# Optimization experiments

Measured on AMD Instinct MI355X. Metric: run time of the kernel, lower is better.

## Reference

```python
import jax, jax.numpy as jnp
import numpy as np

DIM = 1024
NQ = 16
NKV = 4
HD = DIM // NQ  # 64
HID = 2048
E = 8
B, S = 1, 1024
EPS = 1e-6


def rmsnorm(x, w):
    ms = jnp.mean(x * x, axis=-1, keepdims=True)
    return w * (x * jax.lax.rsqrt(ms + EPS))


def rope_tables(seq_len, head_dim):
    inv_freq = 1.0 / (10000.0 ** (jnp.arange(0, head_dim, 2, dtype=jnp.float32) / head_dim))
    t = jnp.arange(seq_len, dtype=jnp.float32)
    freqs = jnp.einsum('i,j->ij', t, inv_freq)  # [S, HD/2]
    return jnp.cos(freqs), jnp.sin(freqs)


def apply_rope(x, cos, sin):
    # x: [B, S, H, HD]; cos/sin: [S, HD/2]
    c = cos[None, :, None, :]
    s = sin[None, :, None, :]
    half = x.shape[-1] // 2
    x1, x2 = x[..., :half], x[..., half:]
    return jnp.concatenate([x1 * c - x2 * s, x1 * s + x2 * c], axis=-1)


def setup_inputs() -> dict:
    key = jax.random.key(0)
    ks = jax.random.split(key, 20)
    sc = lambda fan_in: 1.0 / np.sqrt(fan_in)
    d = {}
    d['x'] = jax.random.normal(ks[0], (B, S, DIM), dtype=jnp.float32)
    d['ln1_w'] = jnp.ones((DIM,), jnp.float32)
    d['ln2_w'] = jnp.ones((DIM,), jnp.float32)
    d['Wq'] = jax.random.normal(ks[1], (DIM, DIM), jnp.float32) * sc(DIM)
    d['bq'] = jnp.zeros((DIM,), jnp.float32)
    d['Wk'] = jax.random.normal(ks[2], (DIM, HD * NKV), jnp.float32) * sc(DIM)
    d['bk'] = jnp.zeros((HD * NKV,), jnp.float32)
    d['Wv'] = jax.random.normal(ks[3], (DIM, HD * NKV), jnp.float32) * sc(DIM)
    d['bv'] = jnp.zeros((HD * NKV,), jnp.float32)
    d['qn_w'] = jnp.ones((HD,), jnp.float32)
    d['kn_w'] = jnp.ones((HD,), jnp.float32)
    d['Wg'] = jax.random.normal(ks[4], (HD, HD), jnp.float32) * sc(HD)
    d['bg'] = jnp.zeros((HD,), jnp.float32)
    d['Wo'] = jax.random.normal(ks[5], (DIM, DIM), jnp.float32) * sc(DIM)
    d['bo'] = jnp.zeros((DIM,), jnp.float32)
    d['Wr'] = jax.random.normal(ks[6], (DIM, E), jnp.float32) * sc(DIM)
    d['br'] = jnp.zeros((E,), jnp.float32)
    d['W1'] = jax.random.normal(ks[7], (E, DIM, 2 * HID), jnp.float32) * sc(DIM)
    d['b1'] = jnp.zeros((E, 2 * HID), jnp.float32)
    d['W2'] = jax.random.normal(ks[8], (E, HID, DIM), jnp.float32) * sc(HID)
    d['b2'] = jnp.zeros((E, DIM), jnp.float32)
    return d


def _forward(x, ln1_w, ln2_w, Wq, bq, Wk, bk, Wv, bv, qn_w, kn_w, Wg, bg, Wo, bo,
             Wr, br, W1, b1, W2, b2):
    batch, seq, _ = x.shape
    cos, sin = rope_tables(seq, HD)

    # --- attention ---
    h = rmsnorm(x, ln1_w)
    q = (h @ Wq + bq).reshape(batch, seq, NQ, HD)
    k = (h @ Wk + bk).reshape(batch, seq, NKV, HD)
    v = (h @ Wv + bv).reshape(batch, seq, NKV, HD)
    q = rmsnorm(apply_rope(q, cos, sin), qn_w)
    k = rmsnorm(apply_rope(k, cos, sin), kn_w)
    rep = NQ // NKV
    k = jnp.repeat(k, rep, axis=2)  # [B,S,NQ,HD]
    v = jnp.repeat(v, rep, axis=2)
    scores = jnp.einsum('bthd,bshd->bhts', q, k) / np.sqrt(HD)
    causal = jnp.tril(jnp.ones((seq, seq), dtype=bool))
    scores = jnp.where(causal[None, None], scores, -jnp.inf)
    attn = jax.nn.softmax(scores, axis=-1)
    out = jnp.einsum('bhts,bshd->bthd', attn, v)
    gate = jax.nn.sigmoid(out @ Wg + bg)
    out = (out * gate).reshape(batch, seq, DIM)
    x = x + out @ Wo + bo

    # --- top-1 MoE (note: output is NOT scaled by router probs) ---
    h2 = rmsnorm(x, ln2_w)
    logits = h2 @ Wr + br  # [B,S,E]
    top1 = jnp.argmax(logits, axis=-1).reshape(-1)  # [T]
    xt = h2.reshape(-1, DIM)  # [T,DIM]
    # dense dispatch: run all experts, gather the chosen one
    u = jnp.einsum('td,edf->tef', xt, W1) + b1  # [T,E,2H]
    u1, u2 = u[..., :HID], u[..., HID:]
    act = u1 * jax.nn.sigmoid(u2)  # SwiGLU
    y_all = jnp.einsum('teh,ehd->ted', act, W2) + b2  # [T,E,DIM]
    y = jnp.take_along_axis(y_all, top1[:, None, None], axis=1)[:, 0, :]
    return x + y.reshape(batch, seq, DIM)


def reference(x, ln1_w, ln2_w, Wq, bq, Wk, bk, Wv, bv, qn_w, kn_w, Wg, bg, Wo, bo,
              Wr, br, W1, b1, W2, b2):
    return _forward(x, ln1_w, ln2_w, Wq, bq, Wk, bk, Wv, bv, qn_w, kn_w,
                    Wg, bg, Wo, bo, Wr, br, W1, b1, W2, b2)
```

## Files before the change

kernel.cpp:

```cpp
#include <hip/hip_runtime.h>
#include <hip/hip_bf16.h>
#include <cstddef>

#define DIM 1024
#define NQ 16
#define NKV 4
#define HD 64
#define HID 2048
#define NE 8
#define SEQ 1024
#define EPSF 1e-6f
#define MAX_TILES 24
#define GST 72

typedef __hip_bfloat16 bf16;
typedef __attribute__((ext_vector_type(8))) short short8;
typedef __attribute__((ext_vector_type(4))) float floatx4;

typedef union { short8 s; unsigned int u[4]; } s8u;

__device__ __forceinline__ unsigned int f2b(float f) {
    union { bf16 b; unsigned short s; } u;
    u.b = __float2bfloat16(f);
    return (unsigned int)u.s;
}
__device__ __forceinline__ unsigned int pk2(float a, float b) {
    return f2b(a) | (f2b(b) << 16);
}

__global__ __launch_bounds__(256) void rmsnorm_kernel(const float* __restrict__ src,
                                                      const float* __restrict__ w,
                                                      float* __restrict__ dst)
{
    int row = blockIdx.x, tid = threadIdx.x;
    __shared__ float red[256];
    float vals[4];
    float sq = 0.f;
    size_t base = (size_t)row * DIM;
    #pragma unroll
    for (int i = 0; i < 4; i++) {
        int idx = tid + i * 256;
        float v = src[base + idx];
        vals[i] = v; sq += v * v;
    }
    red[tid] = sq; __syncthreads();
    for (int s = 128; s > 0; s >>= 1) {
        if (tid < s) red[tid] += red[tid + s];
        __syncthreads();
    }
    float rs = 1.0f / sqrtf(red[0] * (1.0f / DIM) + EPSF);
    #pragma unroll
    for (int i = 0; i < 4; i++) {
        int idx = tid + i * 256;
        dst[base + idx] = w[idx] * vals[i] * rs;
    }
}

__global__ __launch_bounds__(256) void gemm_kernel(
    const float* __restrict__ A, const float* __restrict__ B, const float* __restrict__ bias,
    float* __restrict__ C, const float* __restrict__ resf,
    const int* __restrict__ perm, const int* __restrict__ tile_expert,
    int N, int K, int mode)
{
    __shared__ short As[64 * GST];
    __shared__ short Bs[64 * GST];
    int tid = threadIdx.x;
    int mbase = blockIdx.y * 64, nbase = blockIdx.x * 64;

    size_t Beoff = 0, biasoff = 0;
    if (tile_expert) {
        int e = tile_expert[blockIdx.y];
        if (e < 0) return;
        Beoff = (size_t)e * K * N;
        biasoff = (size_t)e * N;
    }

    int ar = tid >> 4, ak = (tid & 15) << 2;
    int bn = tid & 63, bkk = (tid >> 6) << 4;
    const float* BpBase = B + Beoff + (size_t)bkk * N + nbase + bn;

    int wv = tid >> 6, ln = tid & 63;
    int fm = (wv << 4) + (ln & 15);
    int fn = ln & 15;
    int fk = (ln >> 4) << 3;

    floatx4 acc[4];
    #pragma unroll
    for (int nt = 0; nt < 4; nt++)
        #pragma unroll
        for (int r = 0; r < 4; r++) acc[nt][r] = 0.f;

    float4 apre[4];
    float bpre[16];
    #pragma unroll
    for (int p = 0; p < 4; p++)
        apre[p] = *(const float4*)(A + (size_t)(mbase + (p << 4) + ar) * K + ak);
    #pragma unroll
    for (int i = 0; i < 16; i++)
        bpre[i] = BpBase[(size_t)i * N];

    for (int kt = 0; kt < K; kt += 64) {
        #pragma unroll
        for (int p = 0; p < 4; p++) {
            int m = (p << 4) + ar;
            uint2 wpk; wpk.x = pk2(apre[p].x, apre[p].y); wpk.y = pk2(apre[p].z, apre[p].w);
            *(uint2*)&As[m * GST + ak] = wpk;
        }
        {
            unsigned int u[8];
            #pragma unroll
            for (int i = 0; i < 8; i++) u[i] = pk2(bpre[2 * i], bpre[2 * i + 1]);
            *(uint4*)&Bs[bn * GST + bkk]     = make_uint4(u[0], u[1], u[2], u[3]);
            *(uint4*)&Bs[bn * GST + bkk + 8] = make_uint4(u[4], u[5], u[6], u[7]);
        }
        __syncthreads();

        int kn = kt + 64;
        if (kn < K) {
            #pragma unroll
            for (int p = 0; p < 4; p++)
                apre[p] = *(const float4*)(A + (size_t)(mbase + (p << 4) + ar) * K + kn + ak);
            const float* bp = BpBase + (size_t)kn * N;
            #pragma unroll
            for (int i = 0; i < 16; i++) bpre[i] = bp[(size_t)i * N];
        }

        #pragma unroll
        for (int ks = 0; ks < 2; ks++) {
            short8 af = *(const short8*)&As[fm * GST + (ks << 5) + fk];
            #pragma unroll
            for (int nt = 0; nt < 4; nt++) {
                short8 bf = *(const short8*)&Bs[((nt << 4) + fn) * GST + (ks << 5) + fk];
                acc[nt] = __builtin_amdgcn_mfma_f32_16x16x32_bf16(af, bf, acc[nt], 0, 0, 0);
            }
        }
        __syncthreads();
    }

    int rowb = mbase + (wv << 4) + ((ln >> 4) << 2);
    if (mode == 2) {
        int tk[4];
        #pragma unroll
        for (int r = 0; r < 4; r++) tk[r] = perm[rowb + r];
        #pragma unroll
        for (int nt = 0; nt < 4; nt++) {
            int col = nbase + (nt << 4) + fn;
            float bsv = bias[biasoff + col];
            #pragma unroll
            for (int r = 0; r < 4; r++)
                if (tk[r] >= 0)
                    C[(size_t)tk[r] * N + col] = resf[(size_t)tk[r] * N + col] + acc[nt][r] + bsv;
        }
    } else {
        #pragma unroll
        for (int nt = 0; nt < 4; nt++) {
            int col = nbase + (nt << 4) + fn;
            float bsv = bias[col];
            #pragma unroll
            for (int r = 0; r < 4; r++) {
                float vv = acc[nt][r] + bsv;
                if (mode == 1) vv += resf[(size_t)(rowb + r) * N + col];
                C[(size_t)(rowb + r) * N + col] = vv;
            }
        }
    }
}

__global__ __launch_bounds__(256) void qkv_kernel(
    const float* __restrict__ A,
    const float* __restrict__ Wq, const float* __restrict__ bq,
    const float* __restrict__ Wk, const float* __restrict__ bk,
    const float* __restrict__ Wv, const float* __restrict__ bv,
    float* __restrict__ qo, float* __restrict__ ko, float* __restrict__ vo)
{
    __shared__ short As[64 * GST];
    __shared__ short Bs[64 * GST];
    int tid = threadIdx.x;
    int bx = blockIdx.x;
    int mbase = blockIdx.y * 64;

    const float* B; const float* bias; float* C; int N, nbase;
    if (bx < 16)      { B = Wq; bias = bq; C = qo; N = DIM;      nbase = bx * 64; }
    else if (bx < 20) { B = Wk; bias = bk; C = ko; N = NKV * HD; nbase = (bx - 16) * 64; }
    else              { B = Wv; bias = bv; C = vo; N = NKV * HD; nbase = (bx - 20) * 64; }

    int ar = tid >> 4, ak = (tid & 15) << 2;
    int bn = tid & 63, bkk = (tid >> 6) << 4;
    const float* BpBase = B + (size_t)bkk * N + nbase + bn;

    int wv = tid >> 6, ln = tid & 63;
    int fm = (wv << 4) + (ln & 15);
    int fn = ln & 15;
    int fk = (ln >> 4) << 3;

    floatx4 acc[4];
    #pragma unroll
    for (int nt = 0; nt < 4; nt++)
        #pragma unroll
        for (int r = 0; r < 4; r++) acc[nt][r] = 0.f;

    float4 apre[4];
    float bpre[16];
    #pragma unroll
    for (int p = 0; p < 4; p++)
        apre[p] = *(const float4*)(A + (size_t)(mbase + (p << 4) + ar) * DIM + ak);
    #pragma unroll
    for (int i = 0; i < 16; i++)
        bpre[i] = BpBase[(size_t)i * N];

    for (int kt = 0; kt < DIM; kt += 64) {
        #pragma unroll
        for (int p = 0; p < 4; p++) {
            int m = (p << 4) + ar;
            uint2 wpk; wpk.x = pk2(apre[p].x, apre[p].y); wpk.y = pk2(apre[p].z, apre[p].w);
            *(uint2*)&As[m * GST + ak] = wpk;
        }
        {
            unsigned int u[8];
            #pragma unroll
            for (int i = 0; i < 8; i++) u[i] = pk2(bpre[2 * i], bpre[2 * i + 1]);
            *(uint4*)&Bs[bn * GST + bkk]     = make_uint4(u[0], u[1], u[2], u[3]);
            *(uint4*)&Bs[bn * GST + bkk + 8] = make_uint4(u[4], u[5], u[6], u[7]);
        }
        __syncthreads();

        int kn = kt + 64;
        if (kn < DIM) {
            #pragma unroll
            for (int p = 0; p < 4; p++)
                apre[p] = *(const float4*)(A + (size_t)(mbase + (p << 4) + ar) * DIM + kn + ak);
            const float* bp = BpBase + (size_t)kn * N;
            #pragma unroll
            for (int i = 0; i < 16; i++) bpre[i] = bp[(size_t)i * N];
        }

        #pragma unroll
        for (int ks = 0; ks < 2; ks++) {
            short8 af = *(const short8*)&As[fm * GST + (ks << 5) + fk];
            #pragma unroll
            for (int nt = 0; nt < 4; nt++) {
                short8 bf = *(const short8*)&Bs[((nt << 4) + fn) * GST + (ks << 5) + fk];
                acc[nt] = __builtin_amdgcn_mfma_f32_16x16x32_bf16(af, bf, acc[nt], 0, 0, 0);
            }
        }
        __syncthreads();
    }

    int rowb = mbase + (wv << 4) + ((ln >> 4) << 2);
    #pragma unroll
    for (int nt = 0; nt < 4; nt++) {
        int col = nbase + (nt << 4) + fn;
        float bsv = bias[col];
        #pragma unroll
        for (int r = 0; r < 4; r++)
            C[(size_t)(rowb + r) * N + col] = acc[nt][r] + bsv;
    }
}

__global__ __launch_bounds__(256) void moe1_kernel(
    const float* __restrict__ A,
    const float* __restrict__ W1,
    const float* __restrict__ b1,
    float* __restrict__ act,
    const int* __restrict__ perm,
    const int* __restrict__ tile_expert)
{
    __shared__ short As[64 * GST];
    __shared__ short B1s[64 * GST];
    __shared__ short B2s[64 * GST];
    int tid = threadIdx.x;
    int mbase = blockIdx.y * 64, nbase = blockIdx.x * 64;
    int e = tile_expert[blockIdx.y];
    if (e < 0) return;
    const float* Wp = W1 + (size_t)e * DIM * (2 * HID);
    const float* bp1 = b1 + (size_t)e * (2 * HID);

    int ar = tid >> 4, ak = (tid & 15) << 2;
    int tok[4];
    #pragma unroll
    for (int p = 0; p < 4; p++) tok[p] = perm[mbase + (p << 4) + ar];

    int bn = tid & 63, bkk = (tid >> 6) << 4;
    const float* BpBase = Wp + (size_t)bkk * (2 * HID) + nbase + bn;

    int wv = tid >> 6, ln = tid & 63;
    int fm = (wv << 4) + (ln & 15);
    int fn = ln & 15;
    int fk = (ln >> 4) << 3;

    floatx4 acc1[4], acc2[4];
    #pragma unroll
    for (int nt = 0; nt < 4; nt++)
        #pragma unroll
        for (int r = 0; r < 4; r++) { acc1[nt][r] = 0.f; acc2[nt][r] = 0.f; }

    float4 apre[4];
    float b1pre[16], b2pre[16];
    #pragma unroll
    for (int p = 0; p < 4; p++)
        apre[p] = (tok[p] >= 0)
            ? *(const float4*)(A + (size_t)tok[p] * DIM + ak)
            : make_float4(0.f, 0.f, 0.f, 0.f);
    #pragma unroll
    for (int i = 0; i < 16; i++) {
        b1pre[i] = BpBase[(size_t)i * (2 * HID)];
        b2pre[i] = BpBase[(size_t)i * (2 * HID) + HID];
    }

    for (int kt = 0; kt < DIM; kt += 64) {
        #pragma unroll
        for (int p = 0; p < 4; p++) {
            int m = (p << 4) + ar;
            uint2 wpk; wpk.x = pk2(apre[p].x, apre[p].y); wpk.y = pk2(apre[p].z, apre[p].w);
            *(uint2*)&As[m * GST + ak] = wpk;
        }
        {
            unsigned int u1[8], u2[8];
            #pragma unroll
            for (int i = 0; i < 8; i++) {
                u1[i] = pk2(b1pre[2 * i], b1pre[2 * i + 1]);
                u2[i] = pk2(b2pre[2 * i], b2pre[2 * i + 1]);
            }
            *(uint4*)&B1s[bn * GST + bkk]     = make_uint4(u1[0], u1[1], u1[2], u1[3]);
            *(uint4*)&B1s[bn * GST + bkk + 8] = make_uint4(u1[4], u1[5], u1[6], u1[7]);
            *(uint4*)&B2s[bn * GST + bkk]     = make_uint4(u2[0], u2[1], u2[2], u2[3]);
            *(uint4*)&B2s[bn * GST + bkk + 8] = make_uint4(u2[4], u2[5], u2[6], u2[7]);
        }
        __syncthreads();

        int kn = kt + 64;
        if (kn < DIM) {
            #pragma unroll
            for (int p = 0; p < 4; p++)
                apre[p] = (tok[p] >= 0)
                    ? *(const float4*)(A + (size_t)tok[p] * DIM + kn + ak)
                    : make_float4(0.f, 0.f, 0.f, 0.f);
            const float* bp = BpBase + (size_t)kn * (2 * HID);
            #pragma unroll
            for (int i = 0; i < 16; i++) {
                b1pre[i] = bp[(size_t)i * (2 * HID)];
                b2pre[i] = bp[(size_t)i * (2 * HID) + HID];
            }
        }

        #pragma unroll
        for (int ks = 0; ks < 2; ks++) {
            short8 af = *(const short8*)&As[fm * GST + (ks << 5) + fk];
            #pragma unroll
            for (int nt = 0; nt < 4; nt++) {
                int bo = ((nt << 4) + fn) * GST + (ks << 5) + fk;
                short8 bf1 = *(const short8*)&B1s[bo];
                short8 bf2 = *(const short8*)&B2s[bo];
                acc1[nt] = __builtin_amdgcn_mfma_f32_16x16x32_bf16(af, bf1, acc1[nt], 0, 0, 0);
                acc2[nt] = __builtin_amdgcn_mfma_f32_16x16x32_bf16(af, bf2, acc2[nt], 0, 0, 0);
            }
        }
        __syncthreads();
    }

    int rowb = mbase + (wv << 4) + ((ln >> 4) << 2);
    #pragma unroll
    for (int nt = 0; nt < 4; nt++) {
        int col = nbase + (nt << 4) + fn;
        float bs1 = bp1[col];
        float bs2 = bp1[HID + col];
        #pragma unroll
        for (int r = 0; r < 4; r++) {
            float u1 = acc1[nt][r] + bs1;
            float u2 = acc2[nt][r] + bs2;
            act[(size_t)(rowb + r) * HID + col] = u1 * (1.0f / (1.0f + expf(-u2)));
        }
    }
}

__global__ __launch_bounds__(64) void rope_rms_kernel(float* __restrict__ x,
                                                      const float* __restrict__ w, int nh)
{
    int t = blockIdx.x, h = blockIdx.y, d = threadIdx.x;
    int base = (t * nh + h) * HD;
    int i = d & 31;
    float x1 = x[base + i];
    float x2 = x[base + 32 + i];
    float inv = 1.0f / powf(10000.0f, (float)(2 * i) * (1.0f / HD));
    float fr = (float)t * inv;
    float c = cosf(fr), s = sinf(fr);
    float r = (d < 32) ? (x1 * c - x2 * s) : (x1 * s + x2 * c);
    float sq = r * r;
    #pragma unroll
    for (int m = 32; m >= 1; m >>= 1) sq += __shfl_xor(sq, m);
    float rs = 1.0f / sqrtf(sq * (1.0f / HD) + EPSF);
    __syncthreads();
    x[base + d] = r * rs * w[d];
}

__global__ __launch_bounds__(256) void fattn_kernel(const float* __restrict__ q,
                                                    const float* __restrict__ k,
                                                    const float* __restrict__ v,
                                                    float* __restrict__ o)
{
    __shared__ short lds[2][2][64 * GST];

    int h = blockIdx.x, qt = blockIdx.y;
    int kvh = h >> 2;
    int tid = threadIdx.x;
    int w = tid >> 6, ln = tid & 63;
    int c = ln & 15, g = ln >> 4;
    int qbase = qt * 64;
    const size_t krow = (size_t)NKV * HD;

    short8 qf[2];
    {
        const float* qp = q + ((size_t)(qbase + 16 * w + c) * NQ + h) * HD + 8 * g;
        #pragma unroll
        for (int ks = 0; ks < 2; ks++) {
            float4 a = *(const float4*)(qp + 32 * ks);
            float4 b = *(const float4*)(qp + 32 * ks + 4);
            s8u t;
            t.u[0] = pk2(a.x * 0.125f, a.y * 0.125f);
            t.u[1] = pk2(a.z * 0.125f, a.w * 0.125f);
            t.u[2] = pk2(b.x * 0.125f, b.y * 0.125f);
            t.u[3] = pk2(b.z * 0.125f, b.w * 0.125f);
            qf[ks] = t.s;
        }
    }

    int kr[4], kd4[4];
    #pragma unroll
    for (int i = 0; i < 4; i++) { int f4 = tid + 256 * i; kr[i] = f4 >> 4; kd4[i] = f4 & 15; }
    int vd = tid & 63, vrb = (tid >> 6) << 4;

    float4 kreg[4];
    float vreg[16];
    {
        const float* kb = k + (size_t)kvh * HD;
        #pragma unroll
        for (int i = 0; i < 4; i++)
            kreg[i] = *(const float4*)(kb + (size_t)kr[i] * krow + kd4[i] * 4);
        const float* vb = v + (size_t)kvh * HD + vd;
        #pragma unroll
        for (int i = 0; i < 16; i++)
            vreg[i] = vb[(size_t)(vrb + i) * krow];
    }

    float m_i = -INFINITY, l_i = 0.f;
    floatx4 ot[4];
    #pragma unroll
    for (int mt = 0; mt < 4; mt++)
        #pragma unroll
        for (int r = 0; r < 4; r++) ot[mt][r] = 0.f;

    for (int kt = 0; kt <= qt; kt++) {
        short* KB = lds[kt & 1][0];
        short* VT = lds[kt & 1][1];

        #pragma unroll
        for (int i = 0; i < 4; i++) {
            uint2 wp; wp.x = pk2(kreg[i].x, kreg[i].y); wp.y = pk2(kreg[i].z, kreg[i].w);
            *(uint2*)&KB[kr[i] * GST + kd4[i] * 4] = wp;
        }
        {
            unsigned int u[8];
            #pragma unroll
            for (int i = 0; i < 8; i++) u[i] = pk2(vreg[2 * i], vreg[2 * i + 1]);
            *(uint4*)&VT[vd * GST + vrb]     = make_uint4(u[0], u[1], u[2], u[3]);
            *(uint4*)&VT[vd * GST + vrb + 8] = make_uint4(u[4], u[5], u[6], u[7]);
        }
        __syncthreads();

        if (kt < qt) {
            int kb2 = (kt + 1) * 64;
            const float* kb = k + ((size_t)kb2 * NKV + kvh) * HD;
            #pragma unroll
            for (int i = 0; i < 4; i++)
                kreg[i] = *(const float4*)(kb + (size_t)kr[i] * krow + kd4[i] * 4);
            const float* vp = v + ((size_t)kb2 * NKV + kvh) * HD + vd;
            #pragma unroll
            for (int i = 0; i < 16; i++)
                vreg[i] = vp[(size_t)(vrb + i) * krow];
        }

        float p[4][4];
        #pragma unroll
        for (int mt = 0; mt < 4; mt++) {
            floatx4 s = {0.f, 0.f, 0.f, 0.f};
            #pragma unroll
            for (int ks = 0; ks < 2; ks++) {
                short8 kf = *(const short8*)&KB[(16 * mt + c) * GST + 32 * ks + 8 * g];
                s = __builtin_amdgcn_mfma_f32_16x16x32_bf16(kf, qf[ks], s, 0, 0, 0);
            }
            #pragma unroll
            for (int r = 0; r < 4; r++) p[mt][r] = s[r];
        }

        if (kt == qt) {
            #pragma unroll
            for (int mt = 0; mt < 4; mt++)
                #pragma unroll
                for (int r = 0; r < 4; r++)
                    if (16 * mt + 4 * g + r > 16 * w + c) p[mt][r] = -1e30f;
        }

        float tm = p[0][0];
        #pragma unroll
        for (int mt = 0; mt < 4; mt++)
            #pragma unroll
            for (int r = 0; r < 4; r++) tm = fmaxf(tm, p[mt][r]);
        tm = fmaxf(tm, __shfl_xor(tm, 16));
        tm = fmaxf(tm, __shfl_xor(tm, 32));
        float mn = fmaxf(m_i, tm);
        float alpha = __expf(m_i - mn);
        float ts = 0.f;
        #pragma unroll
        for (int mt = 0; mt < 4; mt++)
            #pragma unroll
            for (int r = 0; r < 4; r++) {
                float e = __expf(p[mt][r] - mn);
                p[mt][r] = e; ts += e;
            }
        ts += __shfl_xor(ts, 16);
        ts += __shfl_xor(ts, 32);
        l_i = alpha * l_i + ts;
        m_i = mn;
        #pragma unroll
        for (int mt = 0; mt < 4; mt++)
            #pragma unroll
            for (int r = 0; r < 4; r++) ot[mt][r] *= alpha;

        unsigned int pd[4][2];
        #pragma unroll
        for (int mt = 0; mt < 4; mt++) {
            pd[mt][0] = pk2(p[mt][0], p[mt][1]);
            pd[mt][1] = pk2(p[mt][2], p[mt][3]);
        }

        int srcA = c + ((ln & 16) << 1);
        int srcB = srcA + 16;
        int gh = g >> 1;
        short8 pf[2];
        #pragma unroll
        for (int ks = 0; ks < 2; ks++) {
            s8u t;
            unsigned int a0 = (unsigned)__shfl((int)pd[2 * ks][0],     srcA);
            unsigned int a1 = (unsigned)__shfl((int)pd[2 * ks + 1][0], srcA);
            t.u[0] = gh ? a1 : a0;
            unsigned int b0 = (unsigned)__shfl((int)pd[2 * ks][1],     srcA);
            unsigned int b1 = (unsigned)__shfl((int)pd[2 * ks + 1][1], srcA);
            t.u[1] = gh ? b1 : b0;
            unsigned int c0 = (unsigned)__shfl((int)pd[2 * ks][0],     srcB);
            unsigned int c1 = (unsigned)__shfl((int)pd[2 * ks + 1][0], srcB);
            t.u[2] = gh ? c1 : c0;
            unsigned int d0 = (unsigned)__shfl((int)pd[2 * ks][1],     srcB);
            unsigned int d1 = (unsigned)__shfl((int)pd[2 * ks + 1][1], srcB);
            t.u[3] = gh ? d1 : d0;
            pf[ks] = t.s;
        }

        #pragma unroll
        for (int mt = 0; mt < 4; mt++) {
            #pragma unroll
            for (int ks = 0; ks < 2; ks++) {
                short8 vf = *(const short8*)&VT[(16 * mt + c) * GST + 32 * ks + 8 * g];
                ot[mt] = __builtin_amdgcn_mfma_f32_16x16x32_bf16(vf, pf[ks], ot[mt], 0, 0, 0);
            }
        }
    }

    __syncthreads();
    float* OT = (float*)lds;
    float rl = 1.0f / l_i;
    #pragma unroll
    for (int mt = 0; mt < 4; mt++)
        #pragma unroll
        for (int r = 0; r < 4; r++)
            OT[(16 * w + c) * 68 + 16 * mt + 4 * g + r] = ot[mt][r] * rl;
    __syncthreads();
    #pragma unroll
    for (int i = 0; i < 4; i++) {
        int idx = tid + 256 * i;
        int rq = idx >> 4, d4 = idx & 15;
        float4 val = *(const float4*)&OT[rq * 68 + d4 * 4];
        *(float4*)(o + ((size_t)(qbase + rq) * NQ + h) * HD + d4 * 4) = val;
    }
}

__global__ __launch_bounds__(64) void gate_kernel(float* __restrict__ o,
                                                  const float* __restrict__ Wg,
                                                  const float* __restrict__ bg)
{
    int t = blockIdx.x, h = blockIdx.y, d = threadIdx.x;
    __shared__ float ao[HD];
    int base = (t * NQ + h) * HD;
    ao[d] = o[base + d];
    __syncthreads();
    float acc = bg[d];
    #pragma unroll 8
    for (int e = 0; e < HD; e++) acc += ao[e] * Wg[e * HD + d];
    float g = 1.0f / (1.0f + expf(-acc));
    o[base + d] = ao[d] * g;
}

__global__ __launch_bounds__(64) void router_kernel(const float* __restrict__ h2,
                                                    const float* __restrict__ Wr,
                                                    const float* __restrict__ br,
                                                    int* __restrict__ top1)
{
    int t = blockIdx.x, lane = threadIdx.x;
    float acc[NE] = {0.f, 0.f, 0.f, 0.f, 0.f, 0.f, 0.f, 0.f};
    for (int d = lane; d < DIM; d += 64) {
        float hv = h2[(size_t)t * DIM + d];
        float4 w0 = *(const float4*)(Wr + (size_t)d * NE);
        float4 w1 = *(const float4*)(Wr + (size_t)d * NE + 4);
        acc[0] += hv * w0.x; acc[1] += hv * w0.y;
        acc[2] += hv * w0.z; acc[3] += hv * w0.w;
        acc[4] += hv * w1.x; acc[5] += hv * w1.y;
        acc[6] += hv * w1.z; acc[7] += hv * w1.w;
    }
    #pragma unroll
    for (int e = 0; e < NE; e++)
        for (int off = 32; off >= 1; off >>= 1) acc[e] += __shfl_down(acc[e], off);
    if (lane == 0) {
        float best = acc[0] + br[0]; int be = 0;
        #pragma unroll
        for (int e = 1; e < NE; e++) {
            float l = acc[e] + br[e];
            if (l > best) { best = l; be = e; }
        }
        top1[t] = be;
    }
}

__global__ __launch_bounds__(64) void bucket_kernel(const int* __restrict__ top1,
                                                    int* __restrict__ perm,
                                                    int* __restrict__ tile_expert)
{
    int lane = threadIdx.x;

    int e_of[16];
    {
        const int4* tp = (const int4*)(top1 + lane * 16);
        #pragma unroll
        for (int c = 0; c < 4; c++) {
            int4 v = tp[c];
            e_of[c * 4 + 0] = v.x & 7;
            e_of[c * 4 + 1] = v.y & 7;
            e_of[c * 4 + 2] = v.z & 7;
            e_of[c * 4 + 3] = v.w & 7;
        }
    }

    int cnt[NE];
    #pragma unroll
    for (int e = 0; e < NE; e++) {
        int c = 0;
        #pragma unroll
        for (int i = 0; i < 16; i++) c += (e_of[i] == e) ? 1 : 0;
        cnt[e] = c;
    }

    int pre[NE];
    #pragma unroll
    for (int e = 0; e < NE; e++) pre[e] = cnt[e];
    #pragma unroll
    for (int off = 1; off < 64; off <<= 1) {
        #pragma unroll
        for (int e = 0; e < NE; e++) {
            int t = __shfl_up(pre[e], off);
            if (lane >= off) pre[e] += t;
        }
    }
    int tot[NE];
    #pragma unroll
    for (int e = 0; e < NE; e++) {
        tot[e] = __shfl(pre[e], 63);
        pre[e] -= cnt[e];
    }

    int off_e[NE + 1];
    off_e[0] = 0;
    #pragma unroll
    for (int e = 0; e < NE; e++)
        off_e[e + 1] = off_e[e] + (((tot[e] + 63) >> 6) << 6);

    if (lane < MAX_TILES) {
        int tb = lane << 6;
        int te = -1;
        #pragma unroll
        for (int e = 0; e < NE; e++)
            if (tb >= off_e[e] && tb < off_e[e + 1]) te = e;
        tile_expert[lane] = te;
    }

    #pragma unroll
    for (int e = 0; e < NE; e++)
        for (int i = off_e[e] + tot[e] + lane; i < off_e[e + 1]; i += 64)
            perm[i] = -1;

    #pragma unroll
    for (int e = 0; e < NE; e++) {
        int pos = off_e[e] + pre[e];
        #pragma unroll
        for (int i = 0; i < 16; i++) {
            if (e_of[i] == e) { perm[pos] = lane * 16 + i; pos++; }
        }
    }
}

extern "C" void kernel_launch(void* const* d_in, const int* in_sizes, int n_in,
                              void* d_out, int out_size, void* d_ws, size_t ws_size,
                              hipStream_t stream)
{
    const float* x    = (const float*)d_in[0];
    const float* ln1w = (const float*)d_in[1];
    const float* ln2w = (const float*)d_in[2];
    const float* Wq   = (const float*)d_in[3];
    const float* bq   = (const float*)d_in[4];
    const float* Wk   = (const float*)d_in[5];
    const float* bk   = (const float*)d_in[6];
    const float* Wv   = (const float*)d_in[7];
    const float* bv   = (const float*)d_in[8];
    const float* qnw  = (const float*)d_in[9];
    const float* knw  = (const float*)d_in[10];
    const float* Wg   = (const float*)d_in[11];
    const float* bg   = (const float*)d_in[12];
    const float* Wo   = (const float*)d_in[13];
    const float* bo   = (const float*)d_in[14];
    const float* Wr   = (const float*)d_in[15];
    const float* br   = (const float*)d_in[16];
    const float* W1   = (const float*)d_in[17];
    const float* b1   = (const float*)d_in[18];
    const float* W2   = (const float*)d_in[19];
    const float* b2   = (const float*)d_in[20];
    float* out = (float*)d_out;
    (void)in_sizes; (void)n_in; (void)out_size; (void)ws_size;

    char* ws = (char*)d_ws;
    float* h    = (float*)(ws);
    float* q    = (float*)(ws + ((size_t)4  << 20));
    float* kbuf = (float*)(ws + ((size_t)8  << 20));
    float* vbuf = (float*)(ws + ((size_t)9  << 20));
    float* ao   = (float*)(ws + ((size_t)10 << 20));
    float* x2   = (float*)(ws);
    float* h2   = (float*)(ws + ((size_t)4  << 20));
    float* act  = (float*)(ws + ((size_t)8  << 20));
    int* top1   = (int*)  (ws + ((size_t)20 << 20));
    int* perm   = top1 + 2048;
    int* texp   = perm + MAX_TILES * 64;

    rmsnorm_kernel<<<SEQ, 256, 0, stream>>>(x, ln1w, h);
    qkv_kernel<<<dim3(24, SEQ / 64), 256, 0, stream>>>(
        h, Wq, bq, Wk, bk, Wv, bv, q, kbuf, vbuf);
    rope_rms_kernel<<<dim3(SEQ, NQ),  64, 0, stream>>>(q,    qnw, NQ);
    rope_rms_kernel<<<dim3(SEQ, NKV), 64, 0, stream>>>(kbuf, knw, NKV);
    fattn_kernel<<<dim3(NQ, SEQ / 64), 256, 0, stream>>>(q, kbuf, vbuf, ao);
    gate_kernel<<<dim3(SEQ, NQ), 64, 0, stream>>>(ao, Wg, bg);
    gemm_kernel<<<dim3(DIM / 64, SEQ / 64), 256, 0, stream>>>(
        ao, Wo, bo, x2, x, nullptr, nullptr, DIM, DIM, 1);
    rmsnorm_kernel<<<SEQ, 256, 0, stream>>>(x2, ln2w, h2);
    router_kernel<<<SEQ, 64, 0, stream>>>(h2, Wr, br, top1);
    bucket_kernel<<<1, 64, 0, stream>>>(top1, perm, texp);
    moe1_kernel<<<dim3(HID / 64, MAX_TILES), 256, 0, stream>>>(
        h2, W1, b1, act, perm, texp);
    gemm_kernel<<<dim3(DIM / 64, MAX_TILES), 256, 0, stream>>>(
        act, W2, b2, out, x2, perm, texp, DIM, HID, 2);
}
```

Measured before the change: 436.9 us.

## Double-buffer GEMM LDS tiles, fuse gate into attention, merge rope launches

Converts the qkv, generic GEMM and MoE up-projection kernels to two shared-memory stages with two register prefetch sets, so one barrier per K-tile can overlap global loads with MFMA. Folds the sigmoid gate projection into the attention epilogue using Wg staged in LDS, removing the separate gate kernel and its extra pass over the attention output. Merges the q and k rope/norm launches into one grid, and relocates workspace offsets for act and routing buffers. Costs are higher register and LDS pressure, which may reduce occupancy.

```diff
diff --git a/kernel.cpp b/kernel.cpp
--- a/kernel.cpp
+++ b/kernel.cpp
@@ -62,8 +62,8 @@
     const int* __restrict__ perm, const int* __restrict__ tile_expert,
     int N, int K, int mode)
 {
-    __shared__ short As[64 * GST];
-    __shared__ short Bs[64 * GST];
+    __shared__ short As[2][64 * GST];
+    __shared__ short Bs[2][64 * GST];
     int tid = threadIdx.x;
     int mbase = blockIdx.y * 64, nbase = blockIdx.x * 64;
 
@@ -90,50 +90,55 @@
         #pragma unroll
         for (int r = 0; r < 4; r++) acc[nt][r] = 0.f;
 
-    float4 apre[4];
-    float bpre[16];
-    #pragma unroll
-    for (int p = 0; p < 4; p++)
-        apre[p] = *(const float4*)(A + (size_t)(mbase + (p << 4) + ar) * K + ak);
-    #pragma unroll
-    for (int i = 0; i < 16; i++)
-        bpre[i] = BpBase[(size_t)i * N];
-
-    for (int kt = 0; kt < K; kt += 64) {
+    float4 aA[4], aB[4];
+    float bA[16], bB[16];
+
+    auto LOAD = [&](int kt2, float4* ap, float* bp_) {
+        #pragma unroll
+        for (int p = 0; p < 4; p++)
+            ap[p] = *(const float4*)(A + (size_t)(mbase + (p << 4) + ar) * K + kt2 + ak);
+        const float* bp = BpBase + (size_t)kt2 * N;
+        #pragma unroll
+        for (int i = 0; i < 16; i++) bp_[i] = bp[(size_t)i * N];
+    };
+    auto STORE = [&](const float4* ap, const float* bp_, short* As_, short* Bs_) {
         #pragma unroll
         for (int p = 0; p < 4; p++) {
             int m = (p << 4) + ar;
-            uint2 wpk; wpk.x = pk2(apre[p].x, apre[p].y); wpk.y = pk2(apre[p].z, apre[p].w);
-            *(uint2*)&As[m * GST + ak] = wpk;
-        }
-        {
-            unsigned int u[8];
-            #pragma unroll
-            for (int i = 0; i < 8; i++) u[i] = pk2(bpre[2 * i], bpre[2 * i + 1]);
-            *(uint4*)&Bs[bn * GST + bkk]     = make_uint4(u[0], u[1], u[2], u[3]);
-            *(uint4*)&Bs[bn * GST + bkk + 8] = make_uint4(u[4], u[5], u[6], u[7]);
-        }
-        __syncthreads();
-
-        int kn = kt + 64;
-        if (kn < K) {
-            #pragma unroll
-            for (int p = 0; p < 4; p++)
-                apre[p] = *(const float4*)(A + (size_t)(mbase + (p << 4) + ar) * K + kn + ak);
-            const float* bp = BpBase + (size_t)kn * N;
-            #pragma unroll
-            for (int i = 0; i < 16; i++) bpre[i] = bp[(size_t)i * N];
-        }
-
+            uint2 wpk; wpk.x = pk2(ap[p].x, ap[p].y); wpk.y = pk2(ap[p].z, ap[p].w);
+            *(uint2*)&As_[m * GST + ak] = wpk;
+        }
+        unsigned int u[8];
+        #pragma unroll
+        for (int i = 0; i < 8; i++) u[i] = pk2(bp_[2 * i], bp_[2 * i + 1]);
+        *(uint4*)&Bs_[bn * GST + bkk]     = make_uint4(u[0], u[1], u[2], u[3]);
+        *(uint4*)&Bs_[bn * GST + bkk + 8] = make_uint4(u[4], u[5], u[6], u[7]);
+    };
+    auto MM = [&](const short* As_, const short* Bs_) {
         #pragma unroll
         for (int ks = 0; ks < 2; ks++) {
-            short8 af = *(const short8*)&As[fm * GST + (ks << 5) + fk];
+            short8 af = *(const short8*)&As_[fm * GST + (ks << 5) + fk];
             #pragma unroll
             for (int nt = 0; nt < 4; nt++) {
-                short8 bf = *(const short8*)&Bs[((nt << 4) + fn) * GST + (ks << 5) + fk];
+                short8 bf = *(const short8*)&Bs_[((nt << 4) + fn) * GST + (ks << 5) + fk];
                 acc[nt] = __builtin_amdgcn_mfma_f32_16x16x32_bf16(af, bf, acc[nt], 0, 0, 0);
             }
         }
+    };
+
+    LOAD(0, aA, bA);
+    STORE(aA, bA, As[0], Bs[0]);
+    LOAD(64, aB, bB);
+    __syncthreads();
+
+    for (int kt = 0; kt < K; kt += 128) {
+        if (kt + 128 < K) LOAD(kt + 128, aA, bA);
+        MM(As[0], Bs[0]);
+        STORE(aB, bB, As[1], Bs[1]);
+        __syncthreads();
+        if (kt + 192 < K) LOAD(kt + 192, aB, bB);
+        MM(As[1], Bs[1]);
+        if (kt + 128 < K) STORE(aA, bA, As[0], Bs[0]);
         __syncthreads();
     }
 
@@ -173,8 +178,8 @@
     const float* __restrict__ Wv, const float* __restrict__ bv,
     float* __restrict__ qo, float* __restrict__ ko, float* __restrict__ vo)
 {
-    __shared__ short As[64 * GST];
-    __shared__ short Bs[64 * GST];
+    __shared__ short As[2][64 * GST];
+    __shared__ short Bs[2][64 * GST];
     int tid = threadIdx.x;
     int bx = blockIdx.x;
     int mbase = blockIdx.y * 64;
@@ -199,50 +204,55 @@
         #pragma unroll
         for (int r = 0; r < 4; r++) acc[nt][r] = 0.f;
 
-    float4 apre[4];
-    float bpre[16];
-    #pragma unroll
-    for (int p = 0; p < 4; p++)
-        apre[p] = *(const float4*)(A + (size_t)(mbase + (p << 4) + ar) * DIM + ak);
-    #pragma unroll
-    for (int i = 0; i < 16; i++)
-        bpre[i] = BpBase[(size_t)i * N];
-
-    for (int kt = 0; kt < DIM; kt += 64) {
+    float4 aA[4], aB[4];
+    float bA[16], bB[16];
+
+    auto LOAD = [&](int kt2, float4* ap, float* bp_) {
+        #pragma unroll
+        for (int p = 0; p < 4; p++)
+            ap[p] = *(const float4*)(A + (size_t)(mbase + (p << 4) + ar) * DIM + kt2 + ak);
+        const float* bp = BpBase + (size_t)kt2 * N;
+        #pragma unroll
+        for (int i = 0; i < 16; i++) bp_[i] = bp[(size_t)i * N];
+    };
+    auto STORE = [&](const float4* ap, const float* bp_, short* As_, short* Bs_) {
         #pragma unroll
         for (int p = 0; p < 4; p++) {
             int m = (p << 4) + ar;
-            uint2 wpk; wpk.x = pk2(apre[p].x, apre[p].y); wpk.y = pk2(apre[p].z, apre[p].w);
-            *(uint2*)&As[m * GST + ak] = wpk;
-        }
-        {
-            unsigned int u[8];
-            #pragma unroll
-            for (int i = 0; i < 8; i++) u[i] = pk2(bpre[2 * i], bpre[2 * i + 1]);
-            *(uint4*)&Bs[bn * GST + bkk]     = make_uint4(u[0], u[1], u[2], u[3]);
-            *(uint4*)&Bs[bn * GST + bkk + 8] = make_uint4(u[4], u[5], u[6], u[7]);
-        }
-        __syncthreads();
-
-        int kn = kt + 64;
-        if (kn < DIM) {
-            #pragma unroll
-            for (int p = 0; p < 4; p++)
-                apre[p] = *(const float4*)(A + (size_t)(mbase + (p << 4) + ar) * DIM + kn + ak);
-            const float* bp = BpBase + (size_t)kn * N;
-            #pragma unroll
-            for (int i = 0; i < 16; i++) bpre[i] = bp[(size_t)i * N];
-        }
-
+            uint2 wpk; wpk.x = pk2(ap[p].x, ap[p].y); wpk.y = pk2(ap[p].z, ap[p].w);
+            *(uint2*)&As_[m * GST + ak] = wpk;
+        }
+        unsigned int u[8];
+        #pragma unroll
+        for (int i = 0; i < 8; i++) u[i] = pk2(bp_[2 * i], bp_[2 * i + 1]);
+        *(uint4*)&Bs_[bn * GST + bkk]     = make_uint4(u[0], u[1], u[2], u[3]);
+        *(uint4*)&Bs_[bn * GST + bkk + 8] = make_uint4(u[4], u[5], u[6], u[7]);
+    };
+    auto MM = [&](const short* As_, const short* Bs_) {
         #pragma unroll
         for (int ks = 0; ks < 2; ks++) {
-            short8 af = *(const short8*)&As[fm * GST + (ks << 5) + fk];
+            short8 af = *(const short8*)&As_[fm * GST + (ks << 5) + fk];
             #pragma unroll
             for (int nt = 0; nt < 4; nt++) {
-                short8 bf = *(const short8*)&Bs[((nt << 4) + fn) * GST + (ks << 5) + fk];
+                short8 bf = *(const short8*)&Bs_[((nt << 4) + fn) * GST + (ks << 5) + fk];
                 acc[nt] = __builtin_amdgcn_mfma_f32_16x16x32_bf16(af, bf, acc[nt], 0, 0, 0);
             }
         }
+    };
+
+    LOAD(0, aA, bA);
+    STORE(aA, bA, As[0], Bs[0]);
+    LOAD(64, aB, bB);
+    __syncthreads();
+
+    for (int kt = 0; kt < DIM; kt += 128) {
+        if (kt + 128 < DIM) LOAD(kt + 128, aA, bA);
+        MM(As[0], Bs[0]);
+        STORE(aB, bB, As[1], Bs[1]);
+        __syncthreads();
+        if (kt + 192 < DIM) LOAD(kt + 192, aB, bB);
+        MM(As[1], Bs[1]);
+        if (kt + 128 < DIM) STORE(aA, bA, As[0], Bs[0]);
         __syncthreads();
     }
 
@@ -265,9 +275,9 @@
     const int* __restrict__ perm,
     const int* __restrict__ tile_expert)
 {
-    __shared__ short As[64 * GST];
-    __shared__ short B1s[64 * GST];
-    __shared__ short B2s[64 * GST];
+    __shared__ short As[2][64 * GST];
+    __shared__ short B1s[2][64 * GST];
+    __shared__ short B2s[2][64 * GST];
     int tid = threadIdx.x;
     int mbase = blockIdx.y * 64, nbase = blockIdx.x * 64;
     int e = tile_expert[blockIdx.y];
@@ -294,67 +304,69 @@
         #pragma unroll
         for (int r = 0; r < 4; r++) { acc1[nt][r] = 0.f; acc2[nt][r] = 0.f; }
 
-    float4 apre[4];
-    float b1pre[16], b2pre[16];
-    #pragma unroll
-    for (int p = 0; p < 4; p++)
-        apre[p] = (tok[p] >= 0)
-            ? *(const float4*)(A + (size_t)tok[p] * DIM + ak)
-            : make_float4(0.f, 0.f, 0.f, 0.f);
-    #pragma unroll
-    for (int i = 0; i < 16; i++) {
-        b1pre[i] = BpBase[(size_t)i * (2 * HID)];
-        b2pre[i] = BpBase[(size_t)i * (2 * HID) + HID];
-    }
-
-    for (int kt = 0; kt < DIM; kt += 64) {
+    float4 aA[4], aB[4];
+    float b1A[16], b1B[16], b2A[16], b2B[16];
+
+    auto LOAD = [&](int kt2, float4* ap, float* b1p, float* b2p) {
+        #pragma unroll
+        for (int p = 0; p < 4; p++)
+            ap[p] = (tok[p] >= 0)
+                ? *(const float4*)(A + (size_t)tok[p] * DIM + kt2 + ak)
+                : make_float4(0.f, 0.f, 0.f, 0.f);
+        const float* bp = BpBase + (size_t)kt2 * (2 * HID);
+        #pragma unroll
+        for (int i = 0; i < 16; i++) {
+            b1p[i] = bp[(size_t)i * (2 * HID)];
+            b2p[i] = bp[(size_t)i * (2 * HID) + HID];
+        }
+    };
+    auto STORE = [&](const float4* ap, const float* b1p, const float* b2p,
+                     short* As_, short* B1s_, short* B2s_) {
         #pragma unroll
         for (int p = 0; p < 4; p++) {
             int m = (p << 4) + ar;
-            uint2 wpk; wpk.x = pk2(apre[p].x, apre[p].y); wpk.y = pk2(apre[p].z, apre[p].w);
-            *(uint2*)&As[m * GST + ak] = wpk;
-        }
-        {
-            unsigned int u1[8], u2[8];
-            #pragma unroll
-            for (int i = 0; i < 8; i++) {
-                u1[i] = pk2(b1pre[2 * i], b1pre[2 * i + 1]);
-                u2[i] = pk2(b2pre[2 * i], b2pre[2 * i + 1]);
-            }
-            *(uint4*)&B1s[bn * GST + bkk]     = make_uint4(u1[0], u1[1], u1[2], u1[3]);
-            *(uint4*)&B1s[bn * GST + bkk + 8] = make_uint4(u1[4], u1[5], u1[6], u1[7]);
-            *(uint4*)&B2s[bn * GST + bkk]     = make_uint4(u2[0], u2[1], u2[2], u2[3]);
-            *(uint4*)&B2s[bn * GST + bkk + 8] = make_uint4(u2[4], u2[5], u2[6], u2[7]);
-        }
-        __syncthreads();
-
-        int kn = kt + 64;
-        if (kn < DIM) {
-            #pragma unroll
-            for (int p = 0; p < 4; p++)
-                apre[p] = (tok[p] >= 0)
-                    ? *(const float4*)(A + (size_t)tok[p] * DIM + kn + ak)
-                    : make_float4(0.f, 0.f, 0.f, 0.f);
-            const float* bp = BpBase + (size_t)kn * (2 * HID);
-            #pragma unroll
-            for (int i = 0; i < 16; i++) {
-                b1pre[i] = bp[(size_t)i * (2 * HID)];
-                b2pre[i] = bp[(size_t)i * (2 * HID) + HID];
-            }
-        }
-
+            uint2 wpk; wpk.x = pk2(ap[p].x, ap[p].y); wpk.y = pk2(ap[p].z, ap[p].w);
+            *(uint2*)&As_[m * GST + ak] = wpk;
+        }
+        unsigned int u1[8], u2[8];
+        #pragma unroll
+        for (int i = 0; i < 8; i++) {
+            u1[i] = pk2(b1p[2 * i], b1p[2 * i + 1]);
+            u2[i] = pk2(b2p[2 * i], b2p[2 * i + 1]);
+        }
+        *(uint4*)&B1s_[bn * GST + bkk]     = make_uint4(u1[0], u1[1], u1[2], u1[3]);
+        *(uint4*)&B1s_[bn * GST + bkk + 8] = make_uint4(u1[4], u1[5], u1[6], u1[7]);
+        *(uint4*)&B2s_[bn * GST + bkk]     = make_uint4(u2[0], u2[1], u2[2], u2[3]);
+        *(uint4*)&B2s_[bn * GST + bkk + 8] = make_uint4(u2[4], u2[5], u2[6], u2[7]);
+    };
+    auto MM = [&](const short* As_, const short* B1s_, const short* B2s_) {
         #pragma unroll
         for (int ks = 0; ks < 2; ks++) {
-            short8 af = *(const short8*)&As[fm * GST + (ks << 5) + fk];
+            short8 af = *(const short8*)&As_[fm * GST + (ks << 5) + fk];
             #pragma unroll
             for (int nt = 0; nt < 4; nt++) {
                 int bo = ((nt << 4) + fn) * GST + (ks << 5) + fk;
-                short8 bf1 = *(const short8*)&B1s[bo];
-                short8 bf2 = *(const short8*)&B2s[bo];
+                short8 bf1 = *(const short8*)&B1s_[bo];
+                short8 bf2 = *(const short8*)&B2s_[bo];
                 acc1[nt] = __builtin_amdgcn_mfma_f32_16x16x32_bf16(af, bf1, acc1[nt], 0, 0, 0);
                 acc2[nt] = __builtin_amdgcn_mfma_f32_16x16x32_bf16(af, bf2, acc2[nt], 0, 0, 0);
             }
         }
+    };
+
+    LOAD(0, aA, b1A, b2A);
+    STORE(aA, b1A, b2A, As[0], B1s[0], B2s[0]);
+    LOAD(64, aB, b1B, b2B);
+    __syncthreads();
+
+    for (int kt = 0; kt < DIM; kt += 128) {
+        if (kt + 128 < DIM) LOAD(kt + 128, aA, b1A, b2A);
+        MM(As[0], B1s[0], B2s[0]);
+        STORE(aB, b1B, b2B, As[1], B1s[1], B2s[1]);
+        __syncthreads();
+        if (kt + 192 < DIM) LOAD(kt + 192, aB, b1B, b2B);
+        MM(As[1], B1s[1], B2s[1]);
+        if (kt + 128 < DIM) STORE(aA, b1A, b2A, As[0], B1s[0], B2s[0]);
         __syncthreads();
     }
 
@@ -373,10 +385,15 @@
     }
 }
 
-__global__ __launch_bounds__(64) void rope_rms_kernel(float* __restrict__ x,
-                                                      const float* __restrict__ w, int nh)
-{
-    int t = blockIdx.x, h = blockIdx.y, d = threadIdx.x;
+__global__ __launch_bounds__(64) void rope_rms_kernel(float* __restrict__ qb,
+                                                      float* __restrict__ kb,
+                                                      const float* __restrict__ qnw,
+                                                      const float* __restrict__ knw)
+{
+    int t = blockIdx.x, hy = blockIdx.y, d = threadIdx.x;
+    float* x; const float* w; int nh, h;
+    if (hy < NQ) { x = qb; w = qnw; nh = NQ;  h = hy; }
+    else         { x = kb; w = knw; nh = NKV; h = hy - NQ; }
     int base = (t * nh + h) * HD;
     int i = d & 31;
     float x1 = x[base + i];
@@ -396,6 +413,8 @@
 __global__ __launch_bounds__(256) void fattn_kernel(const float* __restrict__ q,
                                                     const float* __restrict__ k,
                                                     const float* __restrict__ v,
+                                                    const float* __restrict__ Wg,
+                                                    const float* __restrict__ bg,
                                                     float* __restrict__ o)
 {
     __shared__ short lds[2][2][64 * GST];
@@ -566,37 +585,54 @@
     }
 
     __syncthreads();
-    float* OT = (float*)lds;
+    float* L   = (float*)lds;
+    float* WgS = L + 64 * 68;
+
+    int we = tid >> 2, wd = (tid & 3) << 4;
+    float4 wg4[4];
+    #pragma unroll
+    for (int i = 0; i < 4; i++)
+        wg4[i] = *(const float4*)(Wg + (size_t)we * HD + wd + 4 * i);
+
     float rl = 1.0f / l_i;
     #pragma unroll
     for (int mt = 0; mt < 4; mt++)
         #pragma unroll
         for (int r = 0; r < 4; r++)
-            OT[(16 * w + c) * 68 + 16 * mt + 4 * g + r] = ot[mt][r] * rl;
+            L[(16 * w + c) * 68 + 16 * mt + 4 * g + r] = ot[mt][r] * rl;
+    #pragma unroll
+    for (int i = 0; i < 4; i++)
+        *(float4*)&WgS[we * 68 + wd + 4 * i] = wg4[i];
     __syncthreads();
+
+    int r = tid >> 2, d0 = (tid & 3) << 4;
+    float4 a0 = *(const float4*)(bg + d0);
+    float4 a1 = *(const float4*)(bg + d0 + 4);
+    float4 a2 = *(const float4*)(bg + d0 + 8);
+    float4 a3 = *(const float4*)(bg + d0 + 12);
+    for (int e = 0; e < HD; e++) {
+        float ov = L[r * 68 + e];
+        float4 w0 = *(const float4*)&WgS[e * 68 + d0];
+        float4 w1 = *(const float4*)&WgS[e * 68 + d0 + 4];
+        float4 w2 = *(const float4*)&WgS[e * 68 + d0 + 8];
+        float4 w3 = *(const float4*)&WgS[e * 68 + d0 + 12];
+        a0.x += ov * w0.x; a0.y += ov * w0.y; a0.z += ov * w0.z; a0.w += ov * w0.w;
+        a1.x += ov * w1.x; a1.y += ov * w1.y; a1.z += ov * w1.z; a1.w += ov * w1.w;
+        a2.x += ov * w2.x; a2.y += ov * w2.y; a2.z += ov * w2.z; a2.w += ov * w2.w;
+        a3.x += ov * w3.x; a3.y += ov * w3.y; a3.z += ov * w3.z; a3.w += ov * w3.w;
+    }
+    float* op = o + ((size_t)(qbase + r) * NQ + h) * HD + d0;
+    float4 av[4] = {a0, a1, a2, a3};
     #pragma unroll
     for (int i = 0; i < 4; i++) {
-        int idx = tid + 256 * i;
-        int rq = idx >> 4, d4 = idx & 15;
-        float4 val = *(const float4*)&OT[rq * 68 + d4 * 4];
-        *(float4*)(o + ((size_t)(qbase + rq) * NQ + h) * HD + d4 * 4) = val;
-    }
-}
-
-__global__ __launch_bounds__(64) void gate_kernel(float* __restrict__ o,
-                                                  const float* __restrict__ Wg,
-                                                  const float* __restrict__ bg)
-{
-    int t = blockIdx.x, h = blockIdx.y, d = threadIdx.x;
-    __shared__ float ao[HD];
-    int base = (t * NQ + h) * HD;
-    ao[d] = o[base + d];
-    __syncthreads();
-    float acc = bg[d];
-    #pragma unroll 8
-    for (int e = 0; e < HD; e++) acc += ao[e] * Wg[e * HD + d];
-    float g = 1.0f / (1.0f + expf(-acc));
-    o[base + d] = ao[d] * g;
+        float4 ov4 = *(const float4*)&L[r * 68 + d0 + 4 * i];
+        float4 res;
+        res.x = ov4.x / (1.0f + expf(-av[i].x));
+        res.y = ov4.y / (1.0f + expf(-av[i].y));
+        res.z = ov4.z / (1.0f + expf(-av[i].z));
+        res.w = ov4.w / (1.0f + expf(-av[i].w));
+        *(float4*)(op + 4 * i) = res;
+    }
 }
 
 __global__ __launch_bounds__(64) void router_kernel(const float* __restrict__ h2,
@@ -741,18 +777,16 @@
     float* ao   = (float*)(ws + ((size_t)10 << 20));
     float* x2   = (float*)(ws);
     float* h2   = (float*)(ws + ((size_t)4  << 20));
-    float* act  = (float*)(ws + ((size_t)8  << 20));
-    int* top1   = (int*)  (ws + ((size_t)20 << 20));
+    float* act  = (float*)(ws + ((size_t)24 << 20));
+    int* top1   = (int*)  (ws + ((size_t)44 << 20));
     int* perm   = top1 + 2048;
     int* texp   = perm + MAX_TILES * 64;
 
     rmsnorm_kernel<<<SEQ, 256, 0, stream>>>(x, ln1w, h);
     qkv_kernel<<<dim3(24, SEQ / 64), 256, 0, stream>>>(
         h, Wq, bq, Wk, bk, Wv, bv, q, kbuf, vbuf);
-    rope_rms_kernel<<<dim3(SEQ, NQ),  64, 0, stream>>>(q,    qnw, NQ);
-    rope_rms_kernel<<<dim3(SEQ, NKV), 64, 0, stream>>>(kbuf, knw, NKV);
-    fattn_kernel<<<dim3(NQ, SEQ / 64), 256, 0, stream>>>(q, kbuf, vbuf, ao);
-    gate_kernel<<<dim3(SEQ, NQ), 64, 0, stream>>>(ao, Wg, bg);
+    rope_rms_kernel<<<dim3(SEQ, NQ + NKV), 64, 0, stream>>>(q, kbuf, qnw, knw);
+    fattn_kernel<<<dim3(NQ, SEQ / 64), 256, 0, stream>>>(q, kbuf, vbuf, Wg, bg, ao);
     gemm_kernel<<<dim3(DIM / 64, SEQ / 64), 256, 0, stream>>>(
         ao, Wo, bo, x2, x, nullptr, nullptr, DIM, DIM, 1);
     rmsnorm_kernel<<<SEQ, 256, 0, stream>>>(x2, ln2w, h2);
```

Result: slower. 450.3 us (+3.1%).
